# Kernel tuning notes

Measured on AMD Instinct MI355X. Metric: run time of the kernel, lower is better.

## Reference

```python
import jax, jax.numpy as jnp
import numpy as np

D_MODEL = 1024
NUM_HEADS = 16
D_FF = 4096
EPS = 1e-5


def _linear(x, w, b):
    # torch nn.Linear: y = x @ W^T + b, W is [out, in]
    return jnp.einsum('bld,od->blo', x, w) + b


def _layer_norm(x, g, b):
    mu = jnp.mean(x, axis=-1, keepdims=True)
    var = jnp.mean(jnp.square(x - mu), axis=-1, keepdims=True)
    return (x - mu) / jnp.sqrt(var + EPS) * g + b


def _mha(q, k, v, wq, bq, wk, bk, wv, bv, wo, bo, mask, num_heads):
    B, Lq, D = q.shape
    hd = D // num_heads
    Q = _linear(q, wq, bq).reshape(B, Lq, num_heads, hd).transpose(0, 2, 1, 3)
    K = _linear(k, wk, bk).reshape(B, -1, num_heads, hd).transpose(0, 2, 1, 3)
    V = _linear(v, wv, bv).reshape(B, -1, num_heads, hd).transpose(0, 2, 1, 3)
    scale = jnp.sqrt(jnp.asarray(hd, dtype=q.dtype))
    energy = jnp.einsum('bhqd,bhkd->bhqk', Q, K) / scale  # [B,H,Lq,Lk]
    energy = jnp.where(mask, energy, jnp.asarray(-1e10, dtype=q.dtype))
    attn = jax.nn.softmax(energy, axis=-1)
    x = jnp.einsum('bhqk,bhkd->bhqd', attn, V)
    x = x.transpose(0, 2, 1, 3).reshape(B, Lq, D)
    return _linear(x, wo, bo), attn


def setup_inputs() -> dict:
    key = jax.random.key(0)
    ks = iter(jax.random.split(key, 40))
    B, T, S, D, F = 4, 1024, 1024, D_MODEL, D_FF
    inp = {
        'tgt': jax.random.normal(next(ks), (B, T, D), dtype=jnp.float32),
        'enc_src': jax.random.normal(next(ks), (B, S, D), dtype=jnp.float32),
        'tgt_mask': jnp.tril(jnp.ones((1, 1, T, T), dtype=bool)),
        'src_mask': jnp.ones((1, 1, 1, S), dtype=bool),
    }
    def lin(kk, o, i):
        return jax.random.normal(kk, (o, i), dtype=jnp.float32) * 0.02
    for pfx in ('sa', 'ca'):  # self-attn and cross-attn params
        for nm in ('q', 'k', 'v', 'o'):
            inp[f'{pfx}_w{nm}'] = lin(next(ks), D, D)
            inp[f'{pfx}_b{nm}'] = jnp.zeros((D,), dtype=jnp.float32)
    inp['ff_w1'] = lin(next(ks), F, D)
    inp['ff_b1'] = jnp.zeros((F,), dtype=jnp.float32)
    inp['ff_w2'] = lin(next(ks), D, F)
    inp['ff_b2'] = jnp.zeros((D,), dtype=jnp.float32)
    for i in (1, 2, 3):
        inp[f'ln{i}_g'] = jnp.ones((D,), dtype=jnp.float32)
        inp[f'ln{i}_b'] = jnp.zeros((D,), dtype=jnp.float32)
    return inp


def reference(tgt, enc_src, tgt_mask, src_mask,
              sa_wq, sa_bq, sa_wk, sa_bk, sa_wv, sa_bv, sa_wo, sa_bo,
              ca_wq, ca_bq, ca_wk, ca_bk, ca_wv, ca_bv, ca_wo, ca_bo,
              ff_w1, ff_b1, ff_w2, ff_b2,
              ln1_g, ln1_b, ln2_g, ln2_b, ln3_g, ln3_b):
    # dropout in eval mode (identity)
    _t, _ = _mha(tgt, tgt, tgt, sa_wq, sa_bq, sa_wk, sa_bk, sa_wv, sa_bv,
                 sa_wo, sa_bo, tgt_mask, NUM_HEADS)
    tgt = _layer_norm(tgt + _t, ln1_g, ln1_b)
    _t, attention = _mha(tgt, enc_src, enc_src, ca_wq, ca_bq, ca_wk, ca_bk,
                         ca_wv, ca_bv, ca_wo, ca_bo, src_mask, NUM_HEADS)
    tgt = _layer_norm(tgt + _t, ln2_g, ln2_b)
    _t = _linear(jax.nn.relu(_linear(tgt, ff_w1, ff_b1)), ff_w2, ff_b2)
    tgt = _layer_norm(tgt + _t, ln3_g, ln3_b)
    return tgt, attention
```

## Files before the change

### kernel.cpp

```cpp
#include <hip/hip_runtime.h>
#include <hip/hip_bf16.h>

#define BBATCH 4
#define TT 1024
#define SS 1024
#define DD 1024
#define HH 16
#define HD 64
#define FFD 4096
#define MM (BBATCH*TT)

using f32x4  = __attribute__((ext_vector_type(4))) float;
using s16x8  = __attribute__((ext_vector_type(8))) short;
using bf16x8 = __attribute__((ext_vector_type(8))) __bf16;

__device__ __forceinline__ unsigned short f2b(float f) {
  union { float f; unsigned int u; } x{f};
  unsigned int r = x.u + 0x7FFFu + ((x.u >> 16) & 1u);
  return (unsigned short)(r >> 16);
}

__device__ __forceinline__ void gload16(const void* g, void* l) {
  __builtin_amdgcn_global_load_lds(
      (const __attribute__((address_space(1))) void*)g,
      (__attribute__((address_space(3))) void*)l, 16, 0, 0);
}

__device__ __forceinline__ f32x4 mfma_bf16(s16x8 a, s16x8 b, f32x4 c) {
  return __builtin_amdgcn_mfma_f32_16x16x32_bf16(
      __builtin_bit_cast(bf16x8, a), __builtin_bit_cast(bf16x8, b), c, 0, 0, 0);
}

template <int JT>
__device__ __forceinline__ void gemm_core(
    const unsigned short* __restrict__ Ab, int lda,
    const unsigned short* __restrict__ Bb, int ldb,
    int K, unsigned short* As, unsigned short* Bs, f32x4 (&acc)[4][JT])
{
  const int tid = threadIdx.x, wave = tid >> 6, lane = tid & 63;
  const int r0 = tid >> 2, c0 = (tid & 3) * 8;
  const int wrow = (wave >> 1) * 64, wcol = (wave & 1) * 16 * JT;
  const int q = lane >> 4, rl = lane & 15;
  const s16x8* Av = (const s16x8*)As;
  const s16x8* Bv = (const s16x8*)Bs;

  for (int k0 = 0; k0 < K; k0 += 64) {
#pragma unroll
    for (int s = 0; s < 2; s++) {
      int kk = k0 + s * 32;
      gload16(Ab + (size_t)r0 * lda + kk + c0, As + s * 4096 + wave * 512);
      gload16(Ab + (size_t)(r0 + 64) * lda + kk + c0, As + s * 4096 + wave * 512 + 2048);
      gload16(Bb + (size_t)r0 * ldb + kk + c0, Bs + s * (JT * 1024) + wave * 512);
      if (JT == 4)
        gload16(Bb + (size_t)(r0 + 64) * ldb + kk + c0, Bs + s * (JT * 1024) + wave * 512 + 2048);
    }
    __syncthreads();
#pragma unroll
    for (int s = 0; s < 2; s++) {
      s16x8 af[4], bfr[JT];
#pragma unroll
      for (int t = 0; t < 4; t++) af[t] = Av[s * 512 + (wrow + t * 16 + rl) * 4 + q];
#pragma unroll
      for (int t = 0; t < JT; t++) bfr[t] = Bv[s * (JT * 128) + (wcol + t * 16 + rl) * 4 + q];
#pragma unroll
      for (int i = 0; i < 4; i++)
#pragma unroll
        for (int j = 0; j < JT; j++)
          acc[i][j] = mfma_bf16(af[i], bfr[j], acc[i][j]);
    }
    __syncthreads();
  }
}

template <int EPI, int JT>
__global__ __launch_bounds__(256) void gemm_bt(
    const unsigned short* __restrict__ A, int lda,
    const unsigned short* __restrict__ B, int ldb,
    const float* __restrict__ bias, const float* __restrict__ res,
    float* __restrict__ Cf, unsigned short* __restrict__ Cb, int ldc, int K)
{
  __shared__ __align__(16) unsigned short As[2 * 128 * 32];
  __shared__ __align__(16) unsigned short Bs[2 * JT * 1024];
  const int bm = blockIdx.y, bn = blockIdx.x;
  const int lane = threadIdx.x & 63, wave = threadIdx.x >> 6;
  const int wrow = (wave >> 1) * 64, wcol = (wave & 1) * 16 * JT;
  const int q = lane >> 4, rl = lane & 15;

  f32x4 acc[4][JT];
  f32x4 z = {0.f, 0.f, 0.f, 0.f};
#pragma unroll
  for (int i = 0; i < 4; i++)
#pragma unroll
    for (int j = 0; j < JT; j++) acc[i][j] = z;

  gemm_core<JT>(A + (size_t)bm * 128 * lda, lda,
                B + (size_t)bn * (32 * JT) * ldb, ldb, K, As, Bs, acc);

#pragma unroll
  for (int i = 0; i < 4; i++) {
    int gm0 = bm * 128 + wrow + i * 16 + q * 4;
#pragma unroll
    for (int j = 0; j < JT; j++) {
      int gn = bn * (32 * JT) + wcol + j * 16 + rl;
      float bv = bias[gn];
#pragma unroll
      for (int r = 0; r < 4; r++) {
        size_t off = (size_t)(gm0 + r) * ldc + gn;
        float v = acc[i][j][r];
        if constexpr (EPI == 0) Cb[off] = f2b(v + bv);
        else if constexpr (EPI == 2) Cf[off] = v + bv + res[off];
        else Cb[off] = f2b(fmaxf(v + bv, 0.f));
      }
    }
  }
}

__device__ __forceinline__ void sblock_qk(
    const unsigned short* Qs, const unsigned short* Ks,
    int wrow, int wcol, int q, int rl, f32x4 (&acc)[4][4])
{
  const s16x8* Qv = (const s16x8*)Qs;
  const s16x8* Kv = (const s16x8*)Ks;
  f32x4 z = {0.f, 0.f, 0.f, 0.f};
#pragma unroll
  for (int i = 0; i < 4; i++)
#pragma unroll
    for (int j = 0; j < 4; j++) acc[i][j] = z;
#pragma unroll
  for (int kq = 0; kq < 2; kq++) {
    s16x8 af[4], bf[4];
#pragma unroll
    for (int t = 0; t < 4; t++) af[t] = Qv[kq * 512 + (wrow + t * 16 + rl) * 4 + q];
#pragma unroll
    for (int t = 0; t < 4; t++) bf[t] = Kv[kq * 512 + (wcol + t * 16 + rl) * 4 + q];
#pragma unroll
    for (int i = 0; i < 4; i++)
#pragma unroll
      for (int j = 0; j < 4; j++)
        acc[i][j] = mfma_bf16(af[i], bf[j], acc[i][j]);
  }
}

__global__ __launch_bounds__(256, 2) void flash_sa(
    const unsigned short* __restrict__ Qg, int ldq,
    const unsigned short* __restrict__ Kg, int ldk,
    const unsigned short* __restrict__ Vt,
    unsigned short* __restrict__ Og)
{
  __shared__ __align__(16) unsigned short Qs[2 * 128 * 32];
  __shared__ __align__(16) unsigned short KP[4 * 128 * 40];
  __shared__ __align__(16) unsigned short Vs[4 * 64 * 32];
  __shared__ float red[2][128];

  const int tid = threadIdx.x, wave = tid >> 6, lane = tid & 63;
  const int q = lane >> 4, rl = lane & 15;
  const int bh = blockIdx.y, b = bh >> 4, h = bh & 15;
  const int bm = (bh & 32) ? (7 - blockIdx.x) : blockIdx.x;
  const int wrow = (wave >> 1) * 64, wcol = (wave & 1) * 64;
  const int wc2 = (wave & 1) * 32;
  const int r0 = tid >> 2, c0 = (tid & 3) * 8;

  const unsigned short* Qbase = Qg + ((size_t)b * TT + bm * 128) * ldq + h * HD;
  const unsigned short* Kbase = Kg + (size_t)b * SS * ldk + h * HD;
  const unsigned short* Vbase = Vt + ((size_t)bh << 16);

#pragma unroll
  for (int kq = 0; kq < 2; kq++) {
    gload16(Qbase + (size_t)r0 * ldq + kq * 32 + c0, Qs + kq * 4096 + wave * 512);
    gload16(Qbase + (size_t)(r0 + 64) * ldq + kq * 32 + c0, Qs + kq * 4096 + wave * 512 + 2048);
  }
  const int nch = bm + 1;

  float l_run[4][4];
  f32x4 oacc[4][2];
  f32x4 z = {0.f, 0.f, 0.f, 0.f};
#pragma unroll
  for (int i = 0; i < 4; i++) {
    oacc[i][0] = z; oacc[i][1] = z;
#pragma unroll
    for (int r = 0; r < 4; r++) l_run[i][r] = 0.f;
  }

  for (int c = 0; c < nch; c++) {
    const unsigned short* src = Kbase + (size_t)c * 128 * ldk;
#pragma unroll
    for (int kq = 0; kq < 2; kq++) {
      gload16(src + (size_t)r0 * ldk + kq * 32 + c0, KP + kq * 4096 + wave * 512);
      gload16(src + (size_t)(r0 + 64) * ldk + kq * 32 + c0, KP + kq * 4096 + wave * 512 + 2048);
    }
#pragma unroll
    for (int ks = 0; ks < 4; ks++)
      gload16(Vbase + (size_t)r0 * SS + c * 128 + ks * 32 + c0, Vs + ks * 2048 + wave * 512);
    __syncthreads();

    f32x4 acc[4][4];
    sblock_qk(Qs, KP, wrow, wcol, q, rl, acc);
#pragma unroll
    for (int i = 0; i < 4; i++)
#pragma unroll
      for (int r = 0; r < 4; r++) {
#pragma unroll
        for (int j = 0; j < 4; j++) {
          float v = acc[i][j][r] * 0.125f;
          bool msk = (c == bm) && (wcol + j * 16 + rl) > (wrow + i * 16 + q * 4 + r);
          acc[i][j][r] = msk ? 0.f : __expf(v);
        }
        float s = acc[i][0][r] + acc[i][1][r] + acc[i][2][r] + acc[i][3][r];
#pragma unroll
        for (int off = 1; off < 16; off <<= 1) s += __shfl_xor(s, off);
        l_run[i][r] += s;
      }
    __syncthreads();
#pragma unroll
    for (int i = 0; i < 4; i++)
#pragma unroll
      for (int j = 0; j < 4; j++) {
        int col = wcol + j * 16 + rl;
        int ks = col >> 5, cc = col & 31;
#pragma unroll
        for (int r = 0; r < 4; r++)
          KP[ks * 5120 + (wrow + i * 16 + q * 4 + r) * 40 + cc] = f2b(acc[i][j][r]);
      }
    __syncthreads();
    const s16x8* Pv = (const s16x8*)KP;
    const s16x8* Vv = (const s16x8*)Vs;
#pragma unroll
    for (int ks = 0; ks < 4; ks++) {
      s16x8 af[4], bf[2];
#pragma unroll
      for (int t = 0; t < 4; t++) af[t] = Pv[ks * 640 + (wrow + t * 16 + rl) * 5 + q];
#pragma unroll
      for (int t = 0; t < 2; t++) bf[t] = Vv[ks * 256 + (wc2 + t * 16 + rl) * 4 + q];
#pragma unroll
      for (int i = 0; i < 4; i++)
#pragma unroll
        for (int jt = 0; jt < 2; jt++)
          oacc[i][jt] = mfma_bf16(af[i], bf[jt], oacc[i][jt]);
    }
    __syncthreads();
  }

  if (rl == 0) {
#pragma unroll
    for (int i = 0; i < 4; i++)
#pragma unroll
      for (int r = 0; r < 4; r++)
        red[wave & 1][wrow + i * 16 + q * 4 + r] = l_run[i][r];
  }
  __syncthreads();

#pragma unroll
  for (int i = 0; i < 4; i++) {
#pragma unroll
    for (int r = 0; r < 4; r++) {
      int row = wrow + i * 16 + q * 4 + r;
      float inv = 1.0f / (red[0][row] + red[1][row]);
      int grow = bm * 128 + row;
#pragma unroll
      for (int jt = 0; jt < 2; jt++) {
        int col = h * HD + wc2 + jt * 16 + rl;
        Og[((size_t)b * TT + grow) * DD + col] = f2b(oacc[i][jt][r] * inv);
      }
    }
  }
}

__global__ __launch_bounds__(256, 2) void flash_ca(
    const unsigned short* __restrict__ Qg, int ldq,
    const unsigned short* __restrict__ Kg, int ldk,
    const unsigned short* __restrict__ Vt,
    float* __restrict__ Pout,
    unsigned short* __restrict__ Og)
{
  __shared__ __align__(16) unsigned short Qs[2 * 128 * 32];
  __shared__ __align__(16) unsigned short KP[4 * 128 * 40];
  __shared__ __align__(16) unsigned short Vs[4 * 64 * 32];
  __shared__ float red[2][128];

  const int tid = threadIdx.x, wave = tid >> 6, lane = tid & 63;
  const int q = lane >> 4, rl = lane & 15;
  const int bm = blockIdx.x, bh = blockIdx.y, b = bh >> 4, h = bh & 15;
  const int wrow = (wave >> 1) * 64, wcol = (wave & 1) * 64;
  const int wc2 = (wave & 1) * 32;
  const int r0 = tid >> 2, c0 = (tid & 3) * 8;

  const unsigned short* Qbase = Qg + ((size_t)b * TT + bm * 128) * ldq + h * HD;
  const unsigned short* Kbase = Kg + (size_t)b * SS * ldk + h * HD;
  const unsigned short* Vbase = Vt + ((size_t)bh << 16);

#pragma unroll
  for (int kq = 0; kq < 2; kq++) {
    gload16(Qbase + (size_t)r0 * ldq + kq * 32 + c0, Qs + kq * 4096 + wave * 512);
    gload16(Qbase + (size_t)(r0 + 64) * ldq + kq * 32 + c0, Qs + kq * 4096 + wave * 512 + 2048);
  }

  float l_run[4][4];
#pragma unroll
  for (int i = 0; i < 4; i++)
#pragma unroll
    for (int r = 0; r < 4; r++) l_run[i][r] = 0.f;

  for (int c = 0; c < 8; c++) {
    const unsigned short* src = Kbase + (size_t)c * 128 * ldk;
#pragma unroll
    for (int kq = 0; kq < 2; kq++) {
      gload16(src + (size_t)r0 * ldk + kq * 32 + c0, KP + kq * 4096 + wave * 512);
      gload16(src + (size_t)(r0 + 64) * ldk + kq * 32 + c0, KP + kq * 4096 + wave * 512 + 2048);
    }
    __syncthreads();
    f32x4 acc[4][4];
    sblock_qk(Qs, KP, wrow, wcol, q, rl, acc);
#pragma unroll
    for (int i = 0; i < 4; i++)
#pragma unroll
      for (int r = 0; r < 4; r++) {
        float s = __expf(acc[i][0][r] * 0.125f) + __expf(acc[i][1][r] * 0.125f) +
                  __expf(acc[i][2][r] * 0.125f) + __expf(acc[i][3][r] * 0.125f);
#pragma unroll
        for (int off = 1; off < 16; off <<= 1) s += __shfl_xor(s, off);
        l_run[i][r] += s;
      }
    __syncthreads();
  }
  if (rl == 0) {
#pragma unroll
    for (int i = 0; i < 4; i++)
#pragma unroll
      for (int r = 0; r < 4; r++)
        red[wave & 1][wrow + i * 16 + q * 4 + r] = l_run[i][r];
  }
  __syncthreads();
  float invl[4][4];
#pragma unroll
  for (int i = 0; i < 4; i++)
#pragma unroll
    for (int r = 0; r < 4; r++) {
      int row = wrow + i * 16 + q * 4 + r;
      invl[i][r] = 1.0f / (red[0][row] + red[1][row]);
    }

  f32x4 oacc[4][2];
  f32x4 z = {0.f, 0.f, 0.f, 0.f};
#pragma unroll
  for (int i = 0; i < 4; i++) { oacc[i][0] = z; oacc[i][1] = z; }

  for (int c = 0; c < 8; c++) {
    const unsigned short* src = Kbase + (size_t)c * 128 * ldk;
#pragma unroll
    for (int kq = 0; kq < 2; kq++) {
      gload16(src + (size_t)r0 * ldk + kq * 32 + c0, KP + kq * 4096 + wave * 512);
      gload16(src + (size_t)(r0 + 64) * ldk + kq * 32 + c0, KP + kq * 4096 + wave * 512 + 2048);
    }
#pragma unroll
    for (int ks = 0; ks < 4; ks++)
      gload16(Vbase + (size_t)r0 * SS + c * 128 + ks * 32 + c0, Vs + ks * 2048 + wave * 512);
    __syncthreads();
    f32x4 acc[4][4];
    sblock_qk(Qs, KP, wrow, wcol, q, rl, acc);
#pragma unroll
    for (int i = 0; i < 4; i++)
#pragma unroll
      for (int j = 0; j < 4; j++)
#pragma unroll
        for (int r = 0; r < 4; r++)
          acc[i][j][r] = __expf(acc[i][j][r] * 0.125f) * invl[i][r];
    float* Pb = Pout + ((size_t)bh << 20) +
                ((size_t)(bm * 128 + wrow + q * 4) << 10) + c * 128 + wcol + rl;
#pragma unroll
    for (int i = 0; i < 4; i++)
#pragma unroll
      for (int r = 0; r < 4; r++)
#pragma unroll
        for (int j = 0; j < 4; j++)
          Pb[(size_t)((i * 16 + r) << 10) + j * 16] = acc[i][j][r];
    __syncthreads();
#pragma unroll
    for (int i = 0; i < 4; i++)
#pragma unroll
      for (int j = 0; j < 4; j++) {
        int col = wcol + j * 16 + rl;
        int ks = col >> 5, cc = col & 31;
#pragma unroll
        for (int r = 0; r < 4; r++)
          KP[ks * 5120 + (wrow + i * 16 + q * 4 + r) * 40 + cc] = f2b(acc[i][j][r]);
      }
    __syncthreads();
    const s16x8* Pv = (const s16x8*)KP;
    const s16x8* Vv = (const s16x8*)Vs;
#pragma unroll
    for (int ks = 0; ks < 4; ks++) {
      s16x8 af[4], bf[2];
#pragma unroll
      for (int t = 0; t < 4; t++) af[t] = Pv[ks * 640 + (wrow + t * 16 + rl) * 5 + q];
#pragma unroll
      for (int t = 0; t < 2; t++) bf[t] = Vv[ks * 256 + (wc2 + t * 16 + rl) * 4 + q];
#pragma unroll
      for (int i = 0; i < 4; i++)
#pragma unroll
        for (int jt = 0; jt < 2; jt++)
          oacc[i][jt] = mfma_bf16(af[i], bf[jt], oacc[i][jt]);
    }
    __syncthreads();
  }

#pragma unroll
  for (int i = 0; i < 4; i++)
#pragma unroll
    for (int jt = 0; jt < 2; jt++)
#pragma unroll
      for (int r = 0; r < 4; r++) {
        int row = bm * 128 + wrow + i * 16 + q * 4 + r;
        int col = h * HD + wc2 + jt * 16 + rl;
        Og[((size_t)b * TT + row) * DD + col] = f2b(oacc[i][jt][r]);
      }
}

__global__ __launch_bounds__(256) void transpose_v(
    const unsigned short* __restrict__ V, int ldv, unsigned short* __restrict__ Vt)
{
  __shared__ unsigned short tile[64][68];
  const int bh = blockIdx.z, b = bh >> 4, h = bh & 15;
  const int s0 = blockIdx.x * 64;
  const int tid = threadIdx.x;
#pragma unroll
  for (int i = 0; i < 4; i++) {
    int idx = i * 256 + tid;
    int sl = idx >> 4, d0 = (idx & 15) * 4;
    ushort4 v = *(const ushort4*)&V[((size_t)b * SS + s0 + sl) * ldv + h * HD + d0];
    tile[sl][d0] = v.x; tile[sl][d0 + 1] = v.y; tile[sl][d0 + 2] = v.z; tile[sl][d0 + 3] = v.w;
  }
  __syncthreads();
#pragma unroll
  for (int i = 0; i < 4; i++) {
    int idx = i * 256 + tid;
    int d = idx >> 4, s4 = (idx & 15) * 4;
    ushort4 o = make_ushort4(tile[s4][d], tile[s4 + 1][d], tile[s4 + 2][d], tile[s4 + 3][d]);
    *(ushort4*)&Vt[((size_t)bh * HD + d) * SS + s0 + s4] = o;
  }
}

__global__ __launch_bounds__(256) void ln_k(
    const float* __restrict__ src, const float* __restrict__ g,
    const float* __restrict__ b, float* __restrict__ dstf,
    unsigned short* __restrict__ dstb)
{
  __shared__ float sh[10];
  const size_t row = blockIdx.x;
  const int tid = threadIdx.x;
  float4 v = ((const float4*)(src + (row << 10)))[tid];
  float s = v.x + v.y + v.z + v.w;
  float ss = v.x * v.x + v.y * v.y + v.z * v.z + v.w * v.w;
  for (int o = 32; o; o >>= 1) { s += __shfl_down(s, o); ss += __shfl_down(ss, o); }
  if ((tid & 63) == 0) { sh[tid >> 6] = s; sh[4 + (tid >> 6)] = ss; }
  __syncthreads();
  if (tid == 0) {
    sh[8] = sh[0] + sh[1] + sh[2] + sh[3];
    sh[9] = sh[4] + sh[5] + sh[6] + sh[7];
  }
  __syncthreads();
  const float mean = sh[8] * (1.0f / DD);
  const float var = sh[9] * (1.0f / DD) - mean * mean;
  const float inv = rsqrtf(var + 1e-5f);
  float4 gv = ((const float4*)g)[tid];
  float4 bv = ((const float4*)b)[tid];
  float4 y;
  y.x = (v.x - mean) * inv * gv.x + bv.x;
  y.y = (v.y - mean) * inv * gv.y + bv.y;
  y.z = (v.z - mean) * inv * gv.z + bv.z;
  y.w = (v.w - mean) * inv * gv.w + bv.w;
  if (dstf) ((float4*)(dstf + (row << 10)))[tid] = y;
  if (dstb) {
    ushort4 o = make_ushort4(f2b(y.x), f2b(y.y), f2b(y.z), f2b(y.w));
    ((ushort4*)(dstb + (row << 10)))[tid] = o;
  }
}

struct CvtArgs {
  const float* src[12];
  unsigned short* dst[12];
};

__global__ __launch_bounds__(256) void cvt_all(CvtArgs a) {
  constexpr int st[13] = {0,       1048576, 2097152, 2359296, 2621440,
                          2883584, 3145728, 3407872, 3670016, 3932160,
                          4194304, 5242880, 6291456};
  int i = blockIdx.x * 256 + threadIdx.x;
  int s = 0;
#pragma unroll
  for (int k = 1; k < 12; k++) s += (i >= st[k]) ? 1 : 0;
  int j = i - st[s];
  float4 v = ((const float4*)a.src[s])[j];
  ushort4 o = make_ushort4(f2b(v.x), f2b(v.y), f2b(v.z), f2b(v.w));
  ((ushort4*)a.dst[s])[j] = o;
}

__global__ __launch_bounds__(256) void bias_pack(
    const float* __restrict__ bq, const float* __restrict__ bk, const float* __restrict__ bv,
    const float* __restrict__ bk2, const float* __restrict__ bv2,
    float* __restrict__ bqkv, float* __restrict__ bkv)
{
  int i = blockIdx.x * 256 + threadIdx.x;
  if (i < 1024) bqkv[i] = bq[i];
  else if (i < 2048) bqkv[i] = bk[i - 1024];
  else if (i < 3072) bqkv[i] = bv[i - 2048];
  else if (i < 4096) bkv[i - 3072] = bk2[i - 3072];
  else if (i < 5120) bkv[i - 3072] = bv2[i - 4096 + 1024];
}


extern "C" void kernel_launch(void* const* d_in, const int* in_sizes, int n_in,
                              void* d_out, int out_size, void* d_ws, size_t ws_size,
                              hipStream_t stream)
{
  const float* tgt = (const float*)d_in[0];
  const float* enc = (const float*)d_in[1];
  const float* sa_wq = (const float*)d_in[4];  const float* sa_bq = (const float*)d_in[5];
  const float* sa_wk = (const float*)d_in[6];  const float* sa_bk = (const float*)d_in[7];
  const float* sa_wv = (const float*)d_in[8];  const float* sa_bv = (const float*)d_in[9];
  const float* sa_wo = (const float*)d_in[10]; const float* sa_bo = (const float*)d_in[11];
  const float* ca_wq = (const float*)d_in[12]; const float* ca_bq = (const float*)d_in[13];
  const float* ca_wk = (const float*)d_in[14]; const float* ca_bk = (const float*)d_in[15];
  const float* ca_wv = (const float*)d_in[16]; const float* ca_bv = (const float*)d_in[17];
  const float* ca_wo = (const float*)d_in[18]; const float* ca_bo = (const float*)d_in[19];
  const float* ff_w1 = (const float*)d_in[20]; const float* ff_b1 = (const float*)d_in[21];
  const float* ff_w2 = (const float*)d_in[22]; const float* ff_b2 = (const float*)d_in[23];
  const float* ln1_g = (const float*)d_in[24]; const float* ln1_b = (const float*)d_in[25];
  const float* ln2_g = (const float*)d_in[26]; const float* ln2_b = (const float*)d_in[27];
  const float* ln3_g = (const float*)d_in[28]; const float* ln3_b = (const float*)d_in[29];

  float* out_tgt = (float*)d_out;
  float* out_attn = (float*)d_out + (size_t)MM * DD;

  char* w = (char*)d_ws;
  size_t off = 0;
  auto alloc = [&](size_t bytes) { void* p = w + off; off += (bytes + 255) & ~(size_t)255; return p; };
  unsigned short* Xb   = (unsigned short*)alloc((size_t)MM * DD * 2);
  unsigned short* Eb   = (unsigned short*)alloc((size_t)MM * DD * 2);
  unsigned short* Wq1  = (unsigned short*)alloc((size_t)DD * DD * 2);
  unsigned short* Wk1  = (unsigned short*)alloc((size_t)DD * DD * 2);
  unsigned short* Wv1  = (unsigned short*)alloc((size_t)DD * DD * 2);
  unsigned short* Wo1  = (unsigned short*)alloc((size_t)DD * DD * 2);
  unsigned short* Wq2  = (unsigned short*)alloc((size_t)DD * DD * 2);
  unsigned short* Wk2  = (unsigned short*)alloc((size_t)DD * DD * 2);
  unsigned short* Wv2  = (unsigned short*)alloc((size_t)DD * DD * 2);
  unsigned short* Wo2  = (unsigned short*)alloc((size_t)DD * DD * 2);
  unsigned short* Wf1  = (unsigned short*)alloc((size_t)FFD * DD * 2);
  unsigned short* Wf2  = (unsigned short*)alloc((size_t)DD * FFD * 2);
  unsigned short* QKVb = (unsigned short*)alloc((size_t)MM * 3 * DD * 2);
  unsigned short* KVb  = (unsigned short*)alloc((size_t)MM * 2 * DD * 2);
  unsigned short* Qca  = (unsigned short*)alloc((size_t)MM * DD * 2);
  unsigned short* Vt   = (unsigned short*)alloc((size_t)MM * DD * 2);
  unsigned short* Ob   = (unsigned short*)alloc((size_t)MM * DD * 2);
  float*          res1 = (float*)alloc((size_t)MM * DD * 4);
  unsigned short* t1b  = (unsigned short*)alloc((size_t)MM * DD * 2);
  float*          res2 = (float*)alloc((size_t)MM * DD * 4);
  unsigned short* t2b  = (unsigned short*)alloc((size_t)MM * DD * 2);
  unsigned short* Fb   = (unsigned short*)alloc((size_t)MM * FFD * 2);
  float*          bqkv = (float*)alloc(3072 * 4);
  float*          bkv  = (float*)alloc(2048 * 4);

  CvtArgs ca;
  ca.src[0] = tgt;   ca.dst[0] = Xb;
  ca.src[1] = enc;   ca.dst[1] = Eb;
  ca.src[2] = sa_wq; ca.dst[2] = Wq1;
  ca.src[3] = sa_wk; ca.dst[3] = Wk1;
  ca.src[4] = sa_wv; ca.dst[4] = Wv1;
  ca.src[5] = sa_wo; ca.dst[5] = Wo1;
  ca.src[6] = ca_wq; ca.dst[6] = Wq2;
  ca.src[7] = ca_wk; ca.dst[7] = Wk2;
  ca.src[8] = ca_wv; ca.dst[8] = Wv2;
  ca.src[9] = ca_wo; ca.dst[9] = Wo2;
  ca.src[10] = ff_w1; ca.dst[10] = Wf1;
  ca.src[11] = ff_w2; ca.dst[11] = Wf2;

  bias_pack<<<20, 256, 0, stream>>>(sa_bq, sa_bk, sa_bv, ca_bk, ca_bv, bqkv, bkv);
  cvt_all<<<24576, 256, 0, stream>>>(ca);

  const dim3 gQKV(24, 32);
  const dim3 gKV(16, 32);
  const dim3 gN64(16, 32);
  const dim3 gFF1(32, 32);
  const dim3 gFl(8, 64);
  const dim3 gTr(SS / 64, 1, BBATCH * HH);

  gemm_bt<0, 4><<<gQKV, 256, 0, stream>>>(Xb, DD, Wq1, DD, bqkv, nullptr, nullptr, QKVb, 3 * DD, DD);
  transpose_v<<<gTr, 256, 0, stream>>>(QKVb + 2 * DD, 3 * DD, Vt);
  flash_sa<<<gFl, 256, 0, stream>>>(QKVb, 3 * DD, QKVb + DD, 3 * DD, Vt, Ob);
  gemm_bt<2, 2><<<gN64, 256, 0, stream>>>(Ob, DD, Wo1, DD, sa_bo, tgt, res1, nullptr, DD, DD);
  ln_k<<<MM, 256, 0, stream>>>(res1, ln1_g, ln1_b, res1, t1b);

  gemm_bt<0, 2><<<gN64, 256, 0, stream>>>(t1b, DD, Wq2, DD, ca_bq, nullptr, nullptr, Qca, DD, DD);
  gemm_bt<0, 4><<<gKV, 256, 0, stream>>>(Eb, DD, Wk2, DD, bkv, nullptr, nullptr, KVb, 2 * DD, DD);
  transpose_v<<<gTr, 256, 0, stream>>>(KVb + DD, 2 * DD, Vt);
  flash_ca<<<gFl, 256, 0, stream>>>(Qca, DD, KVb, 2 * DD, Vt, out_attn, Ob);
  gemm_bt<2, 2><<<gN64, 256, 0, stream>>>(Ob, DD, Wo2, DD, ca_bo, res1, res2, nullptr, DD, DD);
  ln_k<<<MM, 256, 0, stream>>>(res2, ln2_g, ln2_b, res2, t2b);

  gemm_bt<3, 4><<<gFF1, 256, 0, stream>>>(t2b, DD, Wf1, DD, ff_b1, nullptr, nullptr, Fb, FFD, DD);
  gemm_bt<2, 2><<<gN64, 256, 0, stream>>>(Fb, FFD, Wf2, FFD, ff_b2, res2, res1, nullptr, DD, FFD);
  ln_k<<<MM, 256, 0, stream>>>(res1, ln3_g, ln3_b, out_tgt, nullptr);
}
```

Measured before the change: 804.0 us.

## Stage cross-attention probabilities through swizzled LDS for coalesced vector stores

Gives P its own XOR-swizzled LDS buffer instead of reusing a padded K buffer. This removes one barrier per chunk and avoids bank conflicts on the P tile. In cross-attention, the full fp32 attention matrix is now written from the LDS tile using 16-byte vector stores per thread rather than scattered 4-byte stores straight from MFMA registers. In exchange, the returned attention probabilities are rounded to bf16 before being widened back to fp32, and LDS use per block grows.

```diff
diff --git a/kernel.cpp b/kernel.cpp
--- a/kernel.cpp
+++ b/kernel.cpp
@@ -20,6 +20,10 @@
   return (unsigned short)(r >> 16);
 }
 
+__device__ __forceinline__ float b2f(unsigned short u) {
+  union { unsigned int i; float f; } x; x.i = (unsigned int)u << 16; return x.f;
+}
+
 __device__ __forceinline__ void gload16(const void* g, void* l) {
   __builtin_amdgcn_global_load_lds(
       (const __attribute__((address_space(1))) void*)g,
@@ -141,6 +145,48 @@
   }
 }
 
+__device__ __forceinline__ void store_ps_swz(
+    unsigned short* Ps, const f32x4 (&acc)[4][4], int wrow, int wcol, int q, int rl)
+{
+#pragma unroll
+  for (int i = 0; i < 4; i++)
+#pragma unroll
+    for (int j = 0; j < 4; j++) {
+      int col = wcol + j * 16 + rl;
+      int ks = col >> 5, cc = col & 31;
+#pragma unroll
+      for (int r = 0; r < 4; r++) {
+        int row = wrow + i * 16 + q * 4 + r;
+        int unit = (row * 4 + (cc >> 3)) ^ ((row >> 1) & 3);
+        Ps[ks * 4096 + unit * 8 + (cc & 7)] = f2b(acc[i][j][r]);
+      }
+    }
+}
+
+__device__ __forceinline__ void pv_swz(
+    const unsigned short* Ps, const unsigned short* Vs,
+    int wrow, int wc2, int q, int rl, f32x4 (&oacc)[4][2])
+{
+  const s16x8* Pv = (const s16x8*)Ps;
+  const s16x8* Vv = (const s16x8*)Vs;
+#pragma unroll
+  for (int ks = 0; ks < 4; ks++) {
+    s16x8 af[4], bf[2];
+#pragma unroll
+    for (int t = 0; t < 4; t++) {
+      int row = wrow + t * 16 + rl;
+      af[t] = Pv[ks * 512 + ((row * 4 + q) ^ ((row >> 1) & 3))];
+    }
+#pragma unroll
+    for (int t = 0; t < 2; t++) bf[t] = Vv[ks * 256 + (wc2 + t * 16 + rl) * 4 + q];
+#pragma unroll
+    for (int i = 0; i < 4; i++)
+#pragma unroll
+      for (int jt = 0; jt < 2; jt++)
+        oacc[i][jt] = mfma_bf16(af[i], bf[jt], oacc[i][jt]);
+  }
+}
+
 __global__ __launch_bounds__(256, 2) void flash_sa(
     const unsigned short* __restrict__ Qg, int ldq,
     const unsigned short* __restrict__ Kg, int ldk,
@@ -148,9 +194,9 @@
     unsigned short* __restrict__ Og)
 {
   __shared__ __align__(16) unsigned short Qs[2 * 128 * 32];
-  __shared__ __align__(16) unsigned short KP[4 * 128 * 40];
+  __shared__ __align__(16) unsigned short Ks[2 * 128 * 32];
   __shared__ __align__(16) unsigned short Vs[4 * 64 * 32];
-  __shared__ float red[2][128];
+  __shared__ __align__(16) unsigned short Ps[4 * 128 * 32];
 
   const int tid = threadIdx.x, wave = tid >> 6, lane = tid & 63;
   const int q = lane >> 4, rl = lane & 15;
@@ -185,8 +231,8 @@
     const unsigned short* src = Kbase + (size_t)c * 128 * ldk;
 #pragma unroll
     for (int kq = 0; kq < 2; kq++) {
-      gload16(src + (size_t)r0 * ldk + kq * 32 + c0, KP + kq * 4096 + wave * 512);
-      gload16(src + (size_t)(r0 + 64) * ldk + kq * 32 + c0, KP + kq * 4096 + wave * 512 + 2048);
+      gload16(src + (size_t)r0 * ldk + kq * 32 + c0, Ks + kq * 4096 + wave * 512);
+      gload16(src + (size_t)(r0 + 64) * ldk + kq * 32 + c0, Ks + kq * 4096 + wave * 512 + 2048);
     }
 #pragma unroll
     for (int ks = 0; ks < 4; ks++)
@@ -194,7 +240,7 @@
     __syncthreads();
 
     f32x4 acc[4][4];
-    sblock_qk(Qs, KP, wrow, wcol, q, rl, acc);
+    sblock_qk(Qs, Ks, wrow, wcol, q, rl, acc);
 #pragma unroll
     for (int i = 0; i < 4; i++)
 #pragma unroll
@@ -210,42 +256,19 @@
         for (int off = 1; off < 16; off <<= 1) s += __shfl_xor(s, off);
         l_run[i][r] += s;
       }
-    __syncthreads();
+    store_ps_swz(Ps, acc, wrow, wcol, q, rl);
+    __syncthreads();
+    pv_swz(Ps, Vs, wrow, wc2, q, rl, oacc);
+    __syncthreads();
+  }
+
+  float* red = (float*)Ps;
+  if (rl == 0) {
 #pragma unroll
     for (int i = 0; i < 4; i++)
 #pragma unroll
-      for (int j = 0; j < 4; j++) {
-        int col = wcol + j * 16 + rl;
-        int ks = col >> 5, cc = col & 31;
-#pragma unroll
-        for (int r = 0; r < 4; r++)
-          KP[ks * 5120 + (wrow + i * 16 + q * 4 + r) * 40 + cc] = f2b(acc[i][j][r]);
-      }
-    __syncthreads();
-    const s16x8* Pv = (const s16x8*)KP;
-    const s16x8* Vv = (const s16x8*)Vs;
-#pragma unroll
-    for (int ks = 0; ks < 4; ks++) {
-      s16x8 af[4], bf[2];
-#pragma unroll
-      for (int t = 0; t < 4; t++) af[t] = Pv[ks * 640 + (wrow + t * 16 + rl) * 5 + q];
-#pragma unroll
-      for (int t = 0; t < 2; t++) bf[t] = Vv[ks * 256 + (wc2 + t * 16 + rl) * 4 + q];
-#pragma unroll
-      for (int i = 0; i < 4; i++)
-#pragma unroll
-        for (int jt = 0; jt < 2; jt++)
-          oacc[i][jt] = mfma_bf16(af[i], bf[jt], oacc[i][jt]);
-    }
-    __syncthreads();
-  }
-
-  if (rl == 0) {
-#pragma unroll
-    for (int i = 0; i < 4; i++)
-#pragma unroll
       for (int r = 0; r < 4; r++)
-        red[wave & 1][wrow + i * 16 + q * 4 + r] = l_run[i][r];
+        red[(wave & 1) * 128 + wrow + i * 16 + q * 4 + r] = l_run[i][r];
   }
   __syncthreads();
 
@@ -254,7 +277,7 @@
 #pragma unroll
     for (int r = 0; r < 4; r++) {
       int row = wrow + i * 16 + q * 4 + r;
-      float inv = 1.0f / (red[0][row] + red[1][row]);
+      float inv = 1.0f / (red[row] + red[128 + row]);
       int grow = bm * 128 + row;
 #pragma unroll
       for (int jt = 0; jt < 2; jt++) {
@@ -273,9 +296,9 @@
     unsigned short* __restrict__ Og)
 {
   __shared__ __align__(16) unsigned short Qs[2 * 128 * 32];
-  __shared__ __align__(16) unsigned short KP[4 * 128 * 40];
+  __shared__ __align__(16) unsigned short Ks[2 * 128 * 32];
   __shared__ __align__(16) unsigned short Vs[4 * 64 * 32];
-  __shared__ float red[2][128];
+  __shared__ __align__(16) unsigned short Ps[4 * 128 * 32];
 
   const int tid = threadIdx.x, wave = tid >> 6, lane = tid & 63;
   const int q = lane >> 4, rl = lane & 15;
@@ -304,12 +327,12 @@
     const unsigned short* src = Kbase + (size_t)c * 128 * ldk;
 #pragma unroll
     for (int kq = 0; kq < 2; kq++) {
-      gload16(src + (size_t)r0 * ldk + kq * 32 + c0, KP + kq * 4096 + wave * 512);
-      gload16(src + (size_t)(r0 + 64) * ldk + kq * 32 + c0, KP + kq * 4096 + wave * 512 + 2048);
+      gload16(src + (size_t)r0 * ldk + kq * 32 + c0, Ks + kq * 4096 + wave * 512);
+      gload16(src + (size_t)(r0 + 64) * ldk + kq * 32 + c0, Ks + kq * 4096 + wave * 512 + 2048);
     }
     __syncthreads();
     f32x4 acc[4][4];
-    sblock_qk(Qs, KP, wrow, wcol, q, rl, acc);
+    sblock_qk(Qs, Ks, wrow, wcol, q, rl, acc);
 #pragma unroll
     for (int i = 0; i < 4; i++)
 #pragma unroll
@@ -322,12 +345,13 @@
       }
     __syncthreads();
   }
+  float* red = (float*)Ps;
   if (rl == 0) {
 #pragma unroll
     for (int i = 0; i < 4; i++)
 #pragma unroll
       for (int r = 0; r < 4; r++)
-        red[wave & 1][wrow + i * 16 + q * 4 + r] = l_run[i][r];
+        red[(wave & 1) * 128 + wrow + i * 16 + q * 4 + r] = l_run[i][r];
   }
   __syncthreads();
   float invl[4][4];
@@ -336,7 +360,7 @@
 #pragma unroll
     for (int r = 0; r < 4; r++) {
       int row = wrow + i * 16 + q * 4 + r;
-      invl[i][r] = 1.0f / (red[0][row] + red[1][row]);
+      invl[i][r] = 1.0f / (red[row] + red[128 + row]);
     }
 
   f32x4 oacc[4][2];
@@ -348,15 +372,15 @@
     const unsigned short* src = Kbase + (size_t)c * 128 * ldk;
 #pragma unroll
     for (int kq = 0; kq < 2; kq++) {
-      gload16(src + (size_t)r0 * ldk + kq * 32 + c0, KP + kq * 4096 + wave * 512);
-      gload16(src + (size_t)(r0 + 64) * ldk + kq * 32 + c0, KP + kq * 4096 + wave * 512 + 2048);
+      gload16(src + (size_t)r0 * ldk + kq * 32 + c0, Ks + kq * 4096 + wave * 512);
+      gload16(src + (size_t)(r0 + 64) * ldk + kq * 32 + c0, Ks + kq * 4096 + wave * 512 + 2048);
     }
 #pragma unroll
     for (int ks = 0; ks < 4; ks++)
       gload16(Vbase + (size_t)r0 * SS + c * 128 + ks * 32 + c0, Vs + ks * 2048 + wave * 512);
     __syncthreads();
     f32x4 acc[4][4];
-    sblock_qk(Qs, KP, wrow, wcol, q, rl, acc);
+    sblock_qk(Qs, Ks, wrow, wcol, q, rl, acc);
 #pragma unroll
     for (int i = 0; i < 4; i++)
 #pragma unroll
@@ -364,42 +388,23 @@
 #pragma unroll
         for (int r = 0; r < 4; r++)
           acc[i][j][r] = __expf(acc[i][j][r] * 0.125f) * invl[i][r];
-    float* Pb = Pout + ((size_t)bh << 20) +
-                ((size_t)(bm * 128 + wrow + q * 4) << 10) + c * 128 + wcol + rl;
-#pragma unroll
-    for (int i = 0; i < 4; i++)
-#pragma unroll
-      for (int r = 0; r < 4; r++)
-#pragma unroll
-        for (int j = 0; j < 4; j++)
-          Pb[(size_t)((i * 16 + r) << 10) + j * 16] = acc[i][j][r];
-    __syncthreads();
-#pragma unroll
-    for (int i = 0; i < 4; i++)
-#pragma unroll
-      for (int j = 0; j < 4; j++) {
-        int col = wcol + j * 16 + rl;
-        int ks = col >> 5, cc = col & 31;
-#pragma unroll
-        for (int r = 0; r < 4; r++)
-          KP[ks * 5120 + (wrow + i * 16 + q * 4 + r) * 40 + cc] = f2b(acc[i][j][r]);
-      }
-    __syncthreads();
-    const s16x8* Pv = (const s16x8*)KP;
-    const s16x8* Vv = (const s16x8*)Vs;
-#pragma unroll
-    for (int ks = 0; ks < 4; ks++) {
-      s16x8 af[4], bf[2];
-#pragma unroll
-      for (int t = 0; t < 4; t++) af[t] = Pv[ks * 640 + (wrow + t * 16 + rl) * 5 + q];
-#pragma unroll
-      for (int t = 0; t < 2; t++) bf[t] = Vv[ks * 256 + (wc2 + t * 16 + rl) * 4 + q];
-#pragma unroll
-      for (int i = 0; i < 4; i++)
-#pragma unroll
-        for (int jt = 0; jt < 2; jt++)
-          oacc[i][jt] = mfma_bf16(af[i], bf[jt], oacc[i][jt]);
-    }
+    store_ps_swz(Ps, acc, wrow, wcol, q, rl);
+    __syncthreads();
+#pragma unroll
+    for (int it = 0; it < 8; it++) {
+      int idx = it * 256 + tid;
+      int ks = idx >> 9, rw = (idx >> 2) & 127, u = idx & 3;
+      s16x8 pv = ((const s16x8*)Ps)[ks * 512 + ((rw * 4 + u) ^ ((rw >> 1) & 3))];
+      float4 lo = make_float4(b2f((unsigned short)pv[0]), b2f((unsigned short)pv[1]),
+                              b2f((unsigned short)pv[2]), b2f((unsigned short)pv[3]));
+      float4 hi = make_float4(b2f((unsigned short)pv[4]), b2f((unsigned short)pv[5]),
+                              b2f((unsigned short)pv[6]), b2f((unsigned short)pv[7]));
+      float* dst = Pout + ((size_t)bh << 20) + ((size_t)(bm * 128 + rw) << 10) +
+                   c * 128 + ks * 32 + u * 8;
+      ((float4*)dst)[0] = lo;
+      ((float4*)dst)[1] = hi;
+    }
+    pv_swz(Ps, Vs, wrow, wc2, q, rl, oacc);
     __syncthreads();
   }
 
```

Measured after the change: 806.4 us. Within noise of the previous version (+0.3%).
